# Kernel optimization log

Measured on AMD Instinct MI355X. Metric: run time of the kernel, lower is better.

The kernel has to match this reference:

```python
import jax, jax.numpy as jnp
import numpy as np

B, S, E_DIM, H_DIM, WID, HGT = 64, 128, 256, 128, 64, 64


def setup_inputs() -> dict:
    key = jax.random.key(0)
    k1, k2, k3, k4 = jax.random.split(key, 4)
    e = jax.random.normal(k1, (B, S, E_DIM), dtype=jnp.float32)
    h = jax.random.normal(k2, (B, H_DIM, WID, HGT), dtype=jnp.float32)
    W = jax.random.normal(k3, (H_DIM, E_DIM), dtype=jnp.float32) * (1.0 / np.sqrt(E_DIM))
    b = jax.random.normal(k4, (H_DIM,), dtype=jnp.float32) * 0.01
    return {"e": e, "h": h, "W": W, "b": b}


def reference(e, h, W, b):
    # Linear: (B, S, e_dim) -> (B, S, h_dim)
    ep = jnp.einsum('bse,de->bsd', e, W) + b
    batch, ch, width, height = h.shape
    hv = h.reshape(batch, ch, width * height)          # (B, D, N)
    # scores s = bmm(e^T_proj, h): (B, S, N)
    s = jnp.einsum('bsd,bdn->bsn', ep, hv)
    # softmax over seq dim (dim=1 in torch)
    beta = jax.nn.softmax(s, axis=1)
    # c = sum_s e[b,d,s] * beta[b,s,n]  -> (B, D, N)  (true batched GEMM)
    c = jnp.einsum('bsd,bsn->bdn', ep, beta)
    return c.reshape(batch, ch, width, height)
```

## Files before the change

### kernel.cpp

```cpp
#include <hip/hip_runtime.h>
#include <math.h>

#define B_ 64
#define S_ 128
#define E_ 256
#define D_ 128
#define N_ 4096

typedef _Float16 f16;
typedef _Float16 f16x8 __attribute__((ext_vector_type(8)));
typedef float f32x4 __attribute__((ext_vector_type(4)));

__device__ __forceinline__ unsigned pack2(f16 a, f16 b) {
    union { f16 h[2]; unsigned u; } x;
    x.h[0] = a; x.h[1] = b; return x.u;
}

__device__ __forceinline__ f32x4 mfma16(f16x8 a, f16x8 b, f32x4 c) {
    return __builtin_amdgcn_mfma_f32_16x16x32_f16(a, b, c, 0, 0, 0);
}

__device__ __forceinline__ void bar_lds() {
    asm volatile("s_waitcnt lgkmcnt(0)" ::: "memory");
    __builtin_amdgcn_s_barrier();
    asm volatile("" ::: "memory");
}

__global__ __launch_bounds__(256) void k1_ep(
    const float* __restrict__ e, const float* __restrict__ W,
    const float* __restrict__ bias,
    unsigned* __restrict__ epA_h, unsigned* __restrict__ epA_l,
    unsigned* __restrict__ epT_h)
{
    __shared__ __align__(16) unsigned char lds[40960];
    f16* ehB = (f16*)lds;
    f16* elB = (f16*)(lds + 4096);
    f16* WhB = (f16*)(lds + 8192);
    f16* WlB = (f16*)(lds + 24576);

    const int t = threadIdx.x;
    const int b  = blockIdx.x >> 2;
    const int s0 = (blockIdx.x & 3) << 5;
    const int wid = t >> 6, lane = t & 63;
    const int l16 = lane & 15, quad = lane >> 4;

    const int se = t >> 3, e8 = t & 7;
    const int dw = t >> 1, half = t & 1;
    const float* egp = e + (size_t)(b * S_ + s0 + se) * E_ + e8 * 8;
    const float* wgp = W + (size_t)dw * E_ + half * 32;
    const int eoff = (se * 128 + e8 * 16) ^ ((se & 7) << 4);
    const int woffb = dw * 128 + half * 64;
    const int wswz = (dw & 7) << 4;

    float4 ve[2], vw[8];
#define K1_LOAD(KC)                                            \
    do {                                                       \
        ve[0] = *(const float4*)(egp + (KC));                  \
        ve[1] = *(const float4*)(egp + (KC) + 4);              \
        _Pragma("unroll")                                      \
        for (int x = 0; x < 8; ++x)                            \
            vw[x] = *(const float4*)(wgp + (KC) + x * 4);      \
    } while (0)

    K1_LOAD(0);

    f32x4 acc[2][2];
#pragma unroll
    for (int mt = 0; mt < 2; ++mt)
#pragma unroll
        for (int nt = 0; nt < 2; ++nt) acc[mt][nt] = (f32x4)0.f;

#pragma unroll 1
    for (int kc = 0; kc < 4; ++kc) {
        {
            f16x8 vh, vl;
#pragma unroll
            for (int x = 0; x < 8; ++x) {
                const float v = (x < 4) ? ((const float*)&ve[0])[x]
                                        : ((const float*)&ve[1])[x - 4];
                const f16 h_ = (f16)v;
                vh[x] = h_; vl[x] = (f16)(v - (float)h_);
            }
            *(f16x8*)((char*)ehB + eoff) = vh;
            *(f16x8*)((char*)elB + eoff) = vl;
        }
#pragma unroll
        for (int g = 0; g < 4; ++g) {
            f16x8 vh, vl;
#pragma unroll
            for (int x = 0; x < 8; ++x) {
                const float v = (x < 4) ? ((const float*)&vw[2 * g])[x]
                                        : ((const float*)&vw[2 * g + 1])[x - 4];
                const f16 h_ = (f16)v;
                vh[x] = h_; vl[x] = (f16)(v - (float)h_);
            }
            const int off = (woffb + g * 16) ^ wswz;
            *(f16x8*)((char*)WhB + off) = vh;
            *(f16x8*)((char*)WlB + off) = vl;
        }
        if (kc < 3) K1_LOAD((kc + 1) * 64);
        bar_lds();

#pragma unroll
        for (int kke = 0; kke < 2; ++kke) {
            const int ebyte = kke * 64 + quad * 16;
            f16x8 ah[2], al[2], bh[2], bl[2];
#pragma unroll
            for (int mt = 0; mt < 2; ++mt) {
                const int row = mt * 16 + l16;
                const int off = (row * 128 + ebyte) ^ ((row & 7) << 4);
                ah[mt] = *(const f16x8*)((const char*)ehB + off);
                al[mt] = *(const f16x8*)((const char*)elB + off);
            }
#pragma unroll
            for (int nt = 0; nt < 2; ++nt) {
                const int dr = (wid << 5) + nt * 16 + l16;
                const int off = (dr * 128 + ebyte) ^ ((dr & 7) << 4);
                bh[nt] = *(const f16x8*)((const char*)WhB + off);
                bl[nt] = *(const f16x8*)((const char*)WlB + off);
            }
#pragma unroll
            for (int mt = 0; mt < 2; ++mt)
#pragma unroll
                for (int nt = 0; nt < 2; ++nt) {
                    acc[mt][nt] = mfma16(ah[mt], bh[nt], acc[mt][nt]);
                    acc[mt][nt] = mfma16(ah[mt], bl[nt], acc[mt][nt]);
                    acc[mt][nt] = mfma16(al[mt], bh[nt], acc[mt][nt]);
                }
        }
        bar_lds();
    }
#undef K1_LOAD

    f16 hi[2][2][4], lo[2][2][4];
#pragma unroll
    for (int nt = 0; nt < 2; ++nt) {
        const int d = (wid << 5) + nt * 16 + l16;
        const float bz = bias[d];
#pragma unroll
        for (int mt = 0; mt < 2; ++mt)
#pragma unroll
            for (int r = 0; r < 4; ++r) {
                const float val = acc[mt][nt][r] + bz;
                const f16 h_ = (f16)val;
                hi[mt][nt][r] = h_;
                lo[mt][nt][r] = (f16)(val - (float)h_);
            }
    }

#pragma unroll
    for (int mt = 0; mt < 2; ++mt)
#pragma unroll
        for (int nt = 0; nt < 2; ++nt) {
            const int d = (wid << 5) + nt * 16 + l16;
            const int sg = s0 + mt * 16 + quad * 4;
            unsigned* p = epT_h + (size_t)(b * D_ + d) * 64 + (sg >> 1);
            p[0] = pack2(hi[mt][nt][0], hi[mt][nt][1]);
            p[1] = pack2(hi[mt][nt][2], hi[mt][nt][3]);
        }

    f16* oAh = (f16*)lds;
    f16* oAl = (f16*)(lds + 8704);
#pragma unroll
    for (int mt = 0; mt < 2; ++mt)
#pragma unroll
        for (int nt = 0; nt < 2; ++nt)
#pragma unroll
            for (int r = 0; r < 4; ++r) {
                const int sl = mt * 16 + quad * 4 + r;
                const int d = (wid << 5) + nt * 16 + l16;
                oAh[sl * 136 + d] = hi[mt][nt][r];
                oAl[sl * 136 + d] = lo[mt][nt][r];
            }
    bar_lds();
    {
        const int sl = t >> 3, j8 = (t & 7) * 8;
        const char* rh = (const char*)oAh + sl * 272 + j8 * 4;
        const char* rl = (const char*)oAl + sl * 272 + j8 * 4;
        uint4* dh = (uint4*)(epA_h + (size_t)(b * S_ + s0 + sl) * 64 + j8);
        uint4* dl = (uint4*)(epA_l + (size_t)(b * S_ + s0 + sl) * 64 + j8);
        dh[0] = *(const uint4*)rh; dh[1] = *(const uint4*)(rh + 16);
        dl[0] = *(const uint4*)rl; dl[1] = *(const uint4*)(rl + 16);
    }
}

__global__ __launch_bounds__(256, 3) void k2_attn(
    const float* __restrict__ h, const f16* __restrict__ epA_h,
    const f16* __restrict__ epA_l, const f16* __restrict__ epT_h,
    float* __restrict__ out)
{
    __shared__ __align__(16) unsigned char hTb[32768];

    f16*   bTp  = (f16*)hTb;
    float* redb = (float*)(hTb + 16384);

    const int phys = blockIdx.x;
    const int L = (phys & 7) * 512 + (phys >> 3);
    const int b  = L >> 6;
    const int n0 = (L & 63) << 6;

    const int t = threadIdx.x;
    const int wid = t >> 6, lane = t & 63;
    const int l16 = lane & 15, quad = lane >> 4;

    const int sn = t & 63;
    float va[32];
    {
        const float* hp = h + (size_t)(b * D_ + wid * 32) * N_ + n0 + sn;
#pragma unroll
        for (int x = 0; x < 32; ++x) va[x] = hp[(size_t)x * N_];
    }
    {
        const int swzn = (sn & 15) << 4;
#pragma unroll
        for (int g = 0; g < 4; ++g) {
            f16x8 vh, vl;
#pragma unroll
            for (int x = 0; x < 8; ++x) {
                const float v = va[g * 8 + x];
                const f16 h_ = (f16)v;
                vh[x] = h_; vl[x] = (f16)(v - (float)h_);
            }
            const int off = (sn * 256 + wid * 64 + g * 16) ^ swzn;
            *(f16x8*)(hTb + off) = vh;
            *(f16x8*)(hTb + 16384 + off) = vl;
        }
    }
    bar_lds();

    const int sb = wid << 5;
    f32x4 acc[2][4];
#pragma unroll
    for (int mt = 0; mt < 2; ++mt)
#pragma unroll
        for (int nt = 0; nt < 4; ++nt) acc[mt][nt] = (f32x4)0.f;

    const f16* Ah = epA_h + (size_t)(b * S_ + sb + l16) * D_ + quad * 8;
    const f16* Al = epA_l + (size_t)(b * S_ + sb + l16) * D_ + quad * 8;
#pragma unroll
    for (int kk = 0; kk < 4; ++kk) {
        const int dcb = kk * 64 + quad * 16;
        f16x8 bh[4], bl[4];
#pragma unroll
        for (int nt = 0; nt < 4; ++nt) {
            const int n = (nt << 4) + l16;
            const int off = (n * 256 + dcb) ^ ((n & 15) << 4);
            bh[nt] = *(const f16x8*)(hTb + off);
            bl[nt] = *(const f16x8*)(hTb + 16384 + off);
        }
#pragma unroll
        for (int mt = 0; mt < 2; ++mt) {
            const f16x8 ah = *(const f16x8*)(Ah + mt * 16 * D_ + kk * 32);
            const f16x8 al = *(const f16x8*)(Al + mt * 16 * D_ + kk * 32);
#pragma unroll
            for (int nt = 0; nt < 4; ++nt) {
                acc[mt][nt] = mfma16(ah, bh[nt], acc[mt][nt]);
                acc[mt][nt] = mfma16(ah, bl[nt], acc[mt][nt]);
                acc[mt][nt] = mfma16(al, bh[nt], acc[mt][nt]);
            }
        }
    }

    float ps[4];
#pragma unroll
    for (int nt = 0; nt < 4; ++nt) {
        float p = 0.f;
#pragma unroll
        for (int mt = 0; mt < 2; ++mt)
#pragma unroll
            for (int r = 0; r < 4; ++r) {
                const float e_ = __expf(acc[mt][nt][r] - 30.f);
                acc[mt][nt][r] = e_;
                p += e_;
            }
        p += __shfl_xor(p, 16);
        p += __shfl_xor(p, 32);
        ps[nt] = p;
    }
    bar_lds();
#pragma unroll
    for (int nt = 0; nt < 4; ++nt)
        if (quad == 0) redb[(((nt << 4) + l16) << 2) + wid] = ps[nt];
    bar_lds();

#pragma unroll
    for (int nt = 0; nt < 4; ++nt) {
        const int n = (nt << 4) + l16;
        const f32x4 s4 = *(const f32x4*)(redb + (n << 2));
        const float inv = 1.f / (s4[0] + s4[1] + s4[2] + s4[3]);
#pragma unroll
        for (int mt = 0; mt < 2; ++mt) {
            uint2 pk;
            pk.x = pack2((f16)(acc[mt][nt][0] * inv),
                         (f16)(acc[mt][nt][1] * inv));
            pk.y = pack2((f16)(acc[mt][nt][2] * inv),
                         (f16)(acc[mt][nt][3] * inv));
            const int bo = (n * 256 + wid * 64 + mt * 32 + quad * 8)
                           ^ ((n & 15) << 4);
            *(uint2*)((char*)bTp + bo) = pk;
        }
    }
    bar_lds();

    const int db = wid << 5;
    f32x4 a2[2][4];
#pragma unroll
    for (int mt = 0; mt < 2; ++mt)
#pragma unroll
        for (int nt = 0; nt < 4; ++nt) a2[mt][nt] = (f32x4)0.f;

    const f16* At = epT_h + (size_t)(b * D_ + db + l16) * S_ + quad * 8;
#pragma unroll
    for (int kk = 0; kk < 4; ++kk) {
        const int scb = kk * 64 + quad * 16;
        f16x8 bb[4];
#pragma unroll
        for (int nt = 0; nt < 4; ++nt) {
            const int n = (nt << 4) + l16;
            const int off = (n * 256 + scb) ^ ((n & 15) << 4);
            bb[nt] = *(const f16x8*)((const char*)bTp + off);
        }
#pragma unroll
        for (int mt = 0; mt < 2; ++mt) {
            const f16x8 av = *(const f16x8*)(At + mt * 16 * S_ + kk * 32);
#pragma unroll
            for (int nt = 0; nt < 4; ++nt)
                a2[mt][nt] = mfma16(av, bb[nt], a2[mt][nt]);
        }
    }

    float* ob = out + (size_t)(b * D_ + db) * N_ + n0;
#pragma unroll
    for (int mt = 0; mt < 2; ++mt)
#pragma unroll
        for (int nt = 0; nt < 4; ++nt)
#pragma unroll
            for (int r = 0; r < 4; ++r)
                ob[(size_t)(mt * 16 + quad * 4 + r) * N_ + (nt << 4) + l16] =
                    a2[mt][nt][r];
}

extern "C" void kernel_launch(void* const* d_in, const int* in_sizes, int n_in,
                              void* d_out, int out_size, void* d_ws, size_t ws_size,
                              hipStream_t stream) {
    const float* e    = (const float*)d_in[0];
    const float* h    = (const float*)d_in[1];
    const float* W    = (const float*)d_in[2];
    const float* bias = (const float*)d_in[3];
    float* out = (float*)d_out;

    unsigned* epA_h = (unsigned*)d_ws;
    unsigned* epA_l = epA_h + (B_ * S_ * D_ / 2);
    unsigned* epT_h = epA_l + (B_ * S_ * D_ / 2);

    hipLaunchKernelGGL(k1_ep, dim3(B_ * 4), dim3(256), 0, stream,
                       e, W, bias, epA_h, epA_l, epT_h);
    hipLaunchKernelGGL(k2_attn, dim3(B_ * 64), dim3(256), 0, stream,
                       h, (const f16*)epA_h, (const f16*)epA_l,
                       (const f16*)epT_h, out);
}
```

Baseline: 299.9 us.

## Make attention blocks persistent over four n-tiles with register-cached ep and h prefetch

Each k2 block now handles four consecutive 64-column n-tiles instead of one, and the grid shrinks by a factor of four. The ep operands (hi, lo and transposed) are loaded into registers once per block and reused across the tiles, so they are no longer re-read from global memory for every tile. The next tile's h values are prefetched into registers while the current tile is computed, and the probability buffer moves to its own LDS region. The costs are much higher register pressure (launch bounds drop to 2 blocks per SM), fewer blocks in flight, and a longer serial loop per block.

```diff
diff --git a/kernel.cpp b/kernel.cpp
--- a/kernel.cpp
+++ b/kernel.cpp
@@ -184,160 +184,174 @@
     }
 }
 
-__global__ __launch_bounds__(256, 3) void k2_attn(
+__global__ __launch_bounds__(256, 2) void k2_attn(
     const float* __restrict__ h, const f16* __restrict__ epA_h,
     const f16* __restrict__ epA_l, const f16* __restrict__ epT_h,
     float* __restrict__ out)
 {
     __shared__ __align__(16) unsigned char hTb[32768];
-
-    f16*   bTp  = (f16*)hTb;
-    float* redb = (float*)(hTb + 16384);
+    __shared__ __align__(16) unsigned char bTb[16384];
 
     const int phys = blockIdx.x;
-    const int L = (phys & 7) * 512 + (phys >> 3);
-    const int b  = L >> 6;
-    const int n0 = (L & 63) << 6;
+    const int L = (phys & 7) * 128 + (phys >> 3);
+    const int b   = L >> 4;
+    const int seg = L & 15;
 
     const int t = threadIdx.x;
     const int wid = t >> 6, lane = t & 63;
     const int l16 = lane & 15, quad = lane >> 4;
-
+    const int sb = wid << 5;
     const int sn = t & 63;
+
+    const f16* Ahp = epA_h + (size_t)(b * S_ + sb + l16) * D_ + quad * 8;
+    const f16* Alp = epA_l + (size_t)(b * S_ + sb + l16) * D_ + quad * 8;
+    const f16* Atp = epT_h + (size_t)(b * D_ + sb + l16) * S_ + quad * 8;
+    f16x8 eah[2][4], eal[2][4], eat[2][4];
+#pragma unroll
+    for (int mt = 0; mt < 2; ++mt)
+#pragma unroll
+        for (int kk = 0; kk < 4; ++kk) {
+            eah[mt][kk] = *(const f16x8*)(Ahp + mt * 16 * D_ + kk * 32);
+            eal[mt][kk] = *(const f16x8*)(Alp + mt * 16 * D_ + kk * 32);
+            eat[mt][kk] = *(const f16x8*)(Atp + mt * 16 * S_ + kk * 32);
+        }
+
+    const float* hpc = h + (size_t)(b * D_ + wid * 32) * N_ + seg * 256 + sn;
+    float* redb = (float*)hTb;
+
     float va[32];
-    {
-        const float* hp = h + (size_t)(b * D_ + wid * 32) * N_ + n0 + sn;
-#pragma unroll
-        for (int x = 0; x < 32; ++x) va[x] = hp[(size_t)x * N_];
-    }
-    {
-        const int swzn = (sn & 15) << 4;
-#pragma unroll
-        for (int g = 0; g < 4; ++g) {
-            f16x8 vh, vl;
-#pragma unroll
-            for (int x = 0; x < 8; ++x) {
-                const float v = va[g * 8 + x];
-                const f16 h_ = (f16)v;
-                vh[x] = h_; vl[x] = (f16)(v - (float)h_);
-            }
-            const int off = (sn * 256 + wid * 64 + g * 16) ^ swzn;
-            *(f16x8*)(hTb + off) = vh;
-            *(f16x8*)(hTb + 16384 + off) = vl;
-        }
-    }
-    bar_lds();
-
-    const int sb = wid << 5;
-    f32x4 acc[2][4];
-#pragma unroll
-    for (int mt = 0; mt < 2; ++mt)
-#pragma unroll
-        for (int nt = 0; nt < 4; ++nt) acc[mt][nt] = (f32x4)0.f;
-
-    const f16* Ah = epA_h + (size_t)(b * S_ + sb + l16) * D_ + quad * 8;
-    const f16* Al = epA_l + (size_t)(b * S_ + sb + l16) * D_ + quad * 8;
-#pragma unroll
-    for (int kk = 0; kk < 4; ++kk) {
-        const int dcb = kk * 64 + quad * 16;
-        f16x8 bh[4], bl[4];
+#pragma unroll
+    for (int x = 0; x < 32; ++x) va[x] = hpc[(size_t)x * N_];
+
+#pragma unroll 1
+    for (int tt = 0; tt < 4; ++tt) {
+        const int n0 = seg * 256 + tt * 64;
+
+        {
+            const int swzn = (sn & 15) << 4;
+#pragma unroll
+            for (int g = 0; g < 4; ++g) {
+                f16x8 vh, vl;
+#pragma unroll
+                for (int x = 0; x < 8; ++x) {
+                    const float v = va[g * 8 + x];
+                    const f16 h_ = (f16)v;
+                    vh[x] = h_; vl[x] = (f16)(v - (float)h_);
+                }
+                const int off = (sn * 256 + wid * 64 + g * 16) ^ swzn;
+                *(f16x8*)(hTb + off) = vh;
+                *(f16x8*)(hTb + 16384 + off) = vl;
+            }
+        }
+        if (tt < 3) {
+            const float* hpn = hpc + (tt + 1) * 64;
+#pragma unroll
+            for (int x = 0; x < 32; ++x) va[x] = hpn[(size_t)x * N_];
+        }
+        bar_lds();
+
+        f32x4 acc[2][4];
+#pragma unroll
+        for (int mt = 0; mt < 2; ++mt)
+#pragma unroll
+            for (int nt = 0; nt < 4; ++nt) acc[mt][nt] = (f32x4)0.f;
+
+#pragma unroll
+        for (int kk = 0; kk < 4; ++kk) {
+            const int dcb = kk * 64 + quad * 16;
+            f16x8 bh[4], bl[4];
+#pragma unroll
+            for (int nt = 0; nt < 4; ++nt) {
+                const int n = (nt << 4) + l16;
+                const int off = (n * 256 + dcb) ^ ((n & 15) << 4);
+                bh[nt] = *(const f16x8*)(hTb + off);
+                bl[nt] = *(const f16x8*)(hTb + 16384 + off);
+            }
+#pragma unroll
+            for (int mt = 0; mt < 2; ++mt) {
+#pragma unroll
+                for (int nt = 0; nt < 4; ++nt) {
+                    acc[mt][nt] = mfma16(eah[mt][kk], bh[nt], acc[mt][nt]);
+                    acc[mt][nt] = mfma16(eah[mt][kk], bl[nt], acc[mt][nt]);
+                    acc[mt][nt] = mfma16(eal[mt][kk], bh[nt], acc[mt][nt]);
+                }
+            }
+        }
+
+        float ps[4];
+#pragma unroll
+        for (int nt = 0; nt < 4; ++nt) {
+            float p = 0.f;
+#pragma unroll
+            for (int mt = 0; mt < 2; ++mt)
+#pragma unroll
+                for (int r = 0; r < 4; ++r) {
+                    const float e_ = __expf(acc[mt][nt][r] - 30.f);
+                    acc[mt][nt][r] = e_;
+                    p += e_;
+                }
+            p += __shfl_xor(p, 16);
+            p += __shfl_xor(p, 32);
+            ps[nt] = p;
+        }
+        bar_lds();
+#pragma unroll
+        for (int nt = 0; nt < 4; ++nt)
+            if (quad == 0) redb[(((nt << 4) + l16) << 2) + wid] = ps[nt];
+        bar_lds();
+
 #pragma unroll
         for (int nt = 0; nt < 4; ++nt) {
             const int n = (nt << 4) + l16;
-            const int off = (n * 256 + dcb) ^ ((n & 15) << 4);
-            bh[nt] = *(const f16x8*)(hTb + off);
-            bl[nt] = *(const f16x8*)(hTb + 16384 + off);
-        }
-#pragma unroll
-        for (int mt = 0; mt < 2; ++mt) {
-            const f16x8 ah = *(const f16x8*)(Ah + mt * 16 * D_ + kk * 32);
-            const f16x8 al = *(const f16x8*)(Al + mt * 16 * D_ + kk * 32);
+            const f32x4 s4 = *(const f32x4*)(redb + (n << 2));
+            const float inv = 1.f / (s4[0] + s4[1] + s4[2] + s4[3]);
+#pragma unroll
+            for (int mt = 0; mt < 2; ++mt) {
+                uint2 pk;
+                pk.x = pack2((f16)(acc[mt][nt][0] * inv),
+                             (f16)(acc[mt][nt][1] * inv));
+                pk.y = pack2((f16)(acc[mt][nt][2] * inv),
+                             (f16)(acc[mt][nt][3] * inv));
+                const int bo = (n * 256 + wid * 64 + mt * 32 + quad * 8)
+                               ^ ((n & 15) << 4);
+                *(uint2*)(bTb + bo) = pk;
+            }
+        }
+        bar_lds();
+
+        f32x4 a2[2][4];
+#pragma unroll
+        for (int mt = 0; mt < 2; ++mt)
+#pragma unroll
+            for (int nt = 0; nt < 4; ++nt) a2[mt][nt] = (f32x4)0.f;
+
+#pragma unroll
+        for (int kk = 0; kk < 4; ++kk) {
+            const int scb = kk * 64 + quad * 16;
+            f16x8 bb[4];
 #pragma unroll
             for (int nt = 0; nt < 4; ++nt) {
-                acc[mt][nt] = mfma16(ah, bh[nt], acc[mt][nt]);
-                acc[mt][nt] = mfma16(ah, bl[nt], acc[mt][nt]);
-                acc[mt][nt] = mfma16(al, bh[nt], acc[mt][nt]);
-            }
-        }
+                const int n = (nt << 4) + l16;
+                const int off = (n * 256 + scb) ^ ((n & 15) << 4);
+                bb[nt] = *(const f16x8*)(bTb + off);
+            }
+#pragma unroll
+            for (int mt = 0; mt < 2; ++mt)
+#pragma unroll
+                for (int nt = 0; nt < 4; ++nt)
+                    a2[mt][nt] = mfma16(eat[mt][kk], bb[nt], a2[mt][nt]);
+        }
+
+        float* ob = out + (size_t)(b * D_ + sb) * N_ + n0;
+#pragma unroll
+        for (int mt = 0; mt < 2; ++mt)
+#pragma unroll
+            for (int nt = 0; nt < 4; ++nt)
+#pragma unroll
+                for (int r = 0; r < 4; ++r)
+                    ob[(size_t)(mt * 16 + quad * 4 + r) * N_ +
+                       (nt << 4) + l16] = a2[mt][nt][r];
     }
-
-    float ps[4];
-#pragma unroll
-    for (int nt = 0; nt < 4; ++nt) {
-        float p = 0.f;
-#pragma unroll
-        for (int mt = 0; mt < 2; ++mt)
-#pragma unroll
-            for (int r = 0; r < 4; ++r) {
-                const float e_ = __expf(acc[mt][nt][r] - 30.f);
-                acc[mt][nt][r] = e_;
-                p += e_;
-            }
-        p += __shfl_xor(p, 16);
-        p += __shfl_xor(p, 32);
-        ps[nt] = p;
-    }
-    bar_lds();
-#pragma unroll
-    for (int nt = 0; nt < 4; ++nt)
-        if (quad == 0) redb[(((nt << 4) + l16) << 2) + wid] = ps[nt];
-    bar_lds();
-
-#pragma unroll
-    for (int nt = 0; nt < 4; ++nt) {
-        const int n = (nt << 4) + l16;
-        const f32x4 s4 = *(const f32x4*)(redb + (n << 2));
-        const float inv = 1.f / (s4[0] + s4[1] + s4[2] + s4[3]);
-#pragma unroll
-        for (int mt = 0; mt < 2; ++mt) {
-            uint2 pk;
-            pk.x = pack2((f16)(acc[mt][nt][0] * inv),
-                         (f16)(acc[mt][nt][1] * inv));
-            pk.y = pack2((f16)(acc[mt][nt][2] * inv),
-                         (f16)(acc[mt][nt][3] * inv));
-            const int bo = (n * 256 + wid * 64 + mt * 32 + quad * 8)
-                           ^ ((n & 15) << 4);
-            *(uint2*)((char*)bTp + bo) = pk;
-        }
-    }
-    bar_lds();
-
-    const int db = wid << 5;
-    f32x4 a2[2][4];
-#pragma unroll
-    for (int mt = 0; mt < 2; ++mt)
-#pragma unroll
-        for (int nt = 0; nt < 4; ++nt) a2[mt][nt] = (f32x4)0.f;
-
-    const f16* At = epT_h + (size_t)(b * D_ + db + l16) * S_ + quad * 8;
-#pragma unroll
-    for (int kk = 0; kk < 4; ++kk) {
-        const int scb = kk * 64 + quad * 16;
-        f16x8 bb[4];
-#pragma unroll
-        for (int nt = 0; nt < 4; ++nt) {
-            const int n = (nt << 4) + l16;
-            const int off = (n * 256 + scb) ^ ((n & 15) << 4);
-            bb[nt] = *(const f16x8*)((const char*)bTp + off);
-        }
-#pragma unroll
-        for (int mt = 0; mt < 2; ++mt) {
-            const f16x8 av = *(const f16x8*)(At + mt * 16 * S_ + kk * 32);
-#pragma unroll
-            for (int nt = 0; nt < 4; ++nt)
-                a2[mt][nt] = mfma16(av, bb[nt], a2[mt][nt]);
-        }
-    }
-
-    float* ob = out + (size_t)(b * D_ + db) * N_ + n0;
-#pragma unroll
-    for (int mt = 0; mt < 2; ++mt)
-#pragma unroll
-        for (int nt = 0; nt < 4; ++nt)
-#pragma unroll
-            for (int r = 0; r < 4; ++r)
-                ob[(size_t)(mt * 16 + quad * 4 + r) * N_ + (nt << 4) + l16] =
-                    a2[mt][nt][r];
 }
 
 extern "C" void kernel_launch(void* const* d_in, const int* in_sizes, int n_in,
@@ -355,7 +369,7 @@
 
     hipLaunchKernelGGL(k1_ep, dim3(B_ * 4), dim3(256), 0, stream,
                        e, W, bias, epA_h, epA_l, epT_h);
-    hipLaunchKernelGGL(k2_attn, dim3(B_ * 64), dim3(256), 0, stream,
+    hipLaunchKernelGGL(k2_attn, dim3(B_ * 16), dim3(256), 0, stream,
                        h, (const f16*)epA_h, (const f16*)epA_l,
                        (const f16*)epT_h, out);
 }
```

After: 310.8 us. 1.04x slower.
